# Kernel optimization log

Hardware: AMD Instinct MI355X
Metric: run time of the kernel (lower is better)

## Reference

```python
import jax, jax.numpy as jnp
import numpy as np
import math

N = 200000      # active voxels
M = 100000      # matched in/out pairs per kernel offset
K = 27          # kernel volume (3x3x3)
CIN = 32
COUT = 64


def setup_inputs() -> dict:
    key = jax.random.key(0)
    k1, k2, k3, k4, k5 = jax.random.split(key, 5)
    input_feat = jax.random.normal(k1, (N, CIN), dtype=jnp.float32)
    input_coord = jax.random.randint(k2, (N, 4), 0, 1024, dtype=jnp.int32)
    input_cmap = jax.random.randint(k3, (N,), 0, N, dtype=jnp.int32)
    input_kmap = jax.random.randint(k4, (K, M, 2), 0, N, dtype=jnp.int32)
    std = 1.0 / math.sqrt(CIN * K)  # reset_parameters: uniform(-std, std)
    kw, kb = jax.random.split(k5)
    kernel = jax.random.uniform(kw, (K, CIN, COUT), dtype=jnp.float32,
                                minval=-std, maxval=std)
    bias = jax.random.uniform(kb, (COUT,), dtype=jnp.float32,
                              minval=-std, maxval=std)
    return {"input_feat": input_feat, "input_coord": input_coord,
            "input_cmap": input_cmap, "input_kmap": input_kmap,
            "kernel": kernel, "bias": bias}


def reference(input_feat, input_coord, input_cmap, input_kmap, kernel, bias):
    # Sparse 3D conv, stride=1: output coords == input coords, n_out = N.
    # For each kernel offset k, the kmap gives (in_idx, out_idx) pairs:
    #   out[out_idx] += in[in_idx] @ kernel[k]
    n_out = input_feat.shape[0]
    in_idx = input_kmap[..., 0]           # [K, M]
    out_idx = input_kmap[..., 1]          # [K, M]
    gathered = input_feat[in_idx]         # [K, M, CIN]  (gather)
    contrib = jnp.einsum('kmi,kio->kmo', gathered, kernel)  # per-offset GEMM
    out = jnp.zeros((n_out, kernel.shape[-1]), dtype=input_feat.dtype)
    out = out.at[out_idx.reshape(-1)].add(contrib.reshape(-1, kernel.shape[-1]))
    out = out + bias
    return out
```

## Files before the change

kernel.cpp:

```cpp
#include <hip/hip_runtime.h>

#define KVOL 27
#define CIN  32
#define COUT 64

__global__ __launch_bounds__(256) void init_out_kernel(float* __restrict__ out,
                                                       const float* __restrict__ bias,
                                                       int total4) {
  int i0 = blockIdx.x * 256 + threadIdx.x;
  float4 b = ((const float4*)bias)[i0 & 15];
  for (int i = i0; i < total4; i += gridDim.x * 256) {
    ((float4*)out)[i] = b;
  }
}

__global__ __launch_bounds__(256) void scatter_conv_kernel(
    const float* __restrict__ feat,
    const int2*  __restrict__ kmap,
    const float* __restrict__ kern,
    float*       __restrict__ out,
    int M) {
  const int k    = blockIdx.y;
  const int lane = threadIdx.x & 63;
  const int wave = threadIdx.x >> 6;

  float w[CIN];
  const float* wk = kern + (size_t)k * CIN * COUT + lane;
#pragma unroll
  for (int i = 0; i < CIN; ++i) w[i] = wk[i * COUT];

  const int2* km = kmap + (size_t)k * M;
  const int nwaves = gridDim.x * 4;

  for (int m = blockIdx.x * 4 + wave; m < M; m += nwaves) {
    int2 pr = km[m];
    const float4* frow = (const float4*)(feat + (size_t)pr.x * CIN);
    float acc = 0.f;
#pragma unroll
    for (int j = 0; j < 8; ++j) {
      float4 v = frow[j];
      acc = fmaf(v.x, w[4 * j + 0], acc);
      acc = fmaf(v.y, w[4 * j + 1], acc);
      acc = fmaf(v.z, w[4 * j + 2], acc);
      acc = fmaf(v.w, w[4 * j + 3], acc);
    }
    atomicAdd(out + (size_t)pr.y * COUT + lane, acc);
  }
}

extern "C" void kernel_launch(void* const* d_in, const int* in_sizes, int n_in,
                              void* d_out, int out_size, void* d_ws, size_t ws_size,
                              hipStream_t stream) {
  const float* feat = (const float*)d_in[0];
  const int2*  kmap = (const int2*)d_in[3];
  const float* kern = (const float*)d_in[4];
  const float* bias = (const float*)d_in[5];
  float* out = (float*)d_out;

  const int N = in_sizes[0] / CIN;
  const int M = in_sizes[3] / (2 * KVOL);

  int total4 = N * (COUT / 4);
  int initBlocks = 2048;
  hipLaunchKernelGGL(init_out_kernel, dim3(initBlocks), dim3(256), 0, stream,
                     out, bias, total4);

  dim3 grid(128, KVOL);
  hipLaunchKernelGGL(scatter_conv_kernel, grid, dim3(256), 0, stream,
                     feat, kmap, kern, out, M);
}
```

Baseline: 831.8 us.

## Bin kernel-map pairs by output row and accumulate per tile in LDS

```diff
diff --git a/kernel.cpp b/kernel.cpp
--- a/kernel.cpp
+++ b/kernel.cpp
@@ -1,50 +1,165 @@
 #include <hip/hip_runtime.h>
+#include <stdint.h>
 
 #define KVOL 27
 #define CIN  32
 #define COUT 64
+#define KPG  3
+#define NGRP 9
+#define RB   64
+#define SCAN_CHUNK 4096
 
-__global__ __launch_bounds__(256) void init_out_kernel(float* __restrict__ out,
-                                                       const float* __restrict__ bias,
-                                                       int total4) {
-  int i0 = blockIdx.x * 256 + threadIdx.x;
-  float4 b = ((const float4*)bias)[i0 & 15];
-  for (int i = i0; i < total4; i += gridDim.x * 256) {
-    ((float4*)out)[i] = b;
+__global__ __launch_bounds__(256) void hist_kernel(const int2* __restrict__ kmap,
+                                                   int* __restrict__ count,
+                                                   int M, int N) {
+  int m = blockIdx.x * 256 + threadIdx.x;
+  int k = blockIdx.y;
+  if (m < M) {
+    int out = kmap[(size_t)k * M + m].y;
+    int w = k / KPG;
+    atomicAdd(&count[w * N + out], 1);
   }
 }
 
-__global__ __launch_bounds__(256) void scatter_conv_kernel(
+__global__ __launch_bounds__(256) void scan_reduce(const int* __restrict__ count,
+                                                   int* __restrict__ partial, int nb) {
+  __shared__ int ws[4];
+  int t = threadIdx.x;
+  int base = blockIdx.x * SCAN_CHUNK + t * 16;
+  int s = 0;
+#pragma unroll
+  for (int i = 0; i < 16; ++i) { int idx = base + i; if (idx < nb) s += count[idx]; }
+  for (int d = 32; d; d >>= 1) s += __shfl_down(s, d);
+  if ((t & 63) == 0) ws[t >> 6] = s;
+  __syncthreads();
+  if (t == 0) partial[blockIdx.x] = ws[0] + ws[1] + ws[2] + ws[3];
+}
+
+__global__ __launch_bounds__(64) void scan_partials(int* __restrict__ partial,
+                                                    int nchunks, int* __restrict__ start_nb) {
+  int lane = threadIdx.x;
+  int run = 0;
+  for (int base = 0; base < nchunks; base += 64) {
+    int i = base + lane;
+    int orig = (i < nchunks) ? partial[i] : 0;
+    int v = orig;
+    for (int d = 1; d < 64; d <<= 1) { int u = __shfl_up(v, d); if (lane >= d) v += u; }
+    if (i < nchunks) partial[i] = run + v - orig;
+    run += __shfl(v, 63);
+  }
+  if (lane == 0) *start_nb = run;
+}
+
+__global__ __launch_bounds__(256) void scan_down(const int* __restrict__ count,
+                                                 const int* __restrict__ partial,
+                                                 int* __restrict__ start,
+                                                 int* __restrict__ cursor, int nb) {
+  __shared__ int wsum[4];
+  int t = threadIdx.x, blk = blockIdx.x;
+  int base = blk * SCAN_CHUNK + t * 16;
+  int v[16]; int s = 0;
+#pragma unroll
+  for (int i = 0; i < 16; ++i) { int idx = base + i; v[i] = (idx < nb) ? count[idx] : 0; s += v[i]; }
+  int lane = t & 63, wv = t >> 6;
+  int sv = s;
+  for (int d = 1; d < 64; d <<= 1) { int u = __shfl_up(sv, d); if (lane >= d) sv += u; }
+  if (lane == 63) wsum[wv] = sv;
+  __syncthreads();
+  int wbase = 0;
+  for (int i = 0; i < wv; ++i) wbase += wsum[i];
+  int prefix = partial[blk] + wbase + (sv - s);
+#pragma unroll
+  for (int i = 0; i < 16; ++i) {
+    int idx = base + i;
+    if (idx < nb) { start[idx] = prefix; cursor[idx] = prefix; }
+    prefix += v[i];
+  }
+}
+
+__global__ __launch_bounds__(256) void scatter_kernel(const int2* __restrict__ kmap,
+                                                      int* __restrict__ cursor,
+                                                      uint32_t* __restrict__ binned,
+                                                      int M, int N) {
+  int m = blockIdx.x * 256 + threadIdx.x;
+  int k = blockIdx.y;
+  if (m < M) {
+    int2 p = kmap[(size_t)k * M + m];
+    int w = k / KPG, kl = k - w * KPG;
+    int pos = atomicAdd(&cursor[w * N + p.y], 1);
+    binned[pos] = (uint32_t)p.x | ((uint32_t)kl << 18) | ((uint32_t)(p.y & (RB - 1)) << 20);
+  }
+}
+
+#define DOT32(F, W, ACC) { _Pragma("unroll") \
+  for (int i_ = 0; i_ < CIN; ++i_) ACC = fmaf((F)[i_], W[i_], ACC); }
+
+#define PROC(E) do { \
+  unsigned in_ = (E) & 0x3FFFFu; \
+  int kl_ = ((E) >> 18) & 3; \
+  int rl_ = (int)((E) >> 20); \
+  const float* f_ = feat + (size_t)in_ * CIN; \
+  float acc_ = 0.f; \
+  if (kl_ == 0)      DOT32(f_, w0, acc_) \
+  else if (kl_ == 1) DOT32(f_, w1, acc_) \
+  else               DOT32(f_, w2, acc_) \
+  atomicAdd(&tile[rl_][c], acc_); \
+} while (0)
+
+__global__ __launch_bounds__(NGRP * 64) void gather_out_kernel(
     const float* __restrict__ feat,
-    const int2*  __restrict__ kmap,
+    const uint32_t* __restrict__ binned,
+    const int* __restrict__ start,
     const float* __restrict__ kern,
-    float*       __restrict__ out,
-    int M) {
-  const int k    = blockIdx.y;
-  const int lane = threadIdx.x & 63;
-  const int wave = threadIdx.x >> 6;
+    const float* __restrict__ bias,
+    float* __restrict__ out,
+    int N) {
+  __shared__ float tile[RB][COUT];
+  const int w  = threadIdx.x >> 6;
+  const int c  = threadIdx.x & 63;
+  const int R0 = blockIdx.x * RB;
 
-  float w[CIN];
-  const float* wk = kern + (size_t)k * CIN * COUT + lane;
+  for (int i = threadIdx.x; i < RB * COUT; i += NGRP * 64) ((float*)tile)[i] = 0.f;
+
+  float w0[CIN], w1[CIN], w2[CIN];
+  {
+    const float* kb = kern + (size_t)(w * KPG) * CIN * COUT + c;
 #pragma unroll
-  for (int i = 0; i < CIN; ++i) w[i] = wk[i * COUT];
+    for (int i = 0; i < CIN; ++i) w0[i] = kb[i * COUT];
+#pragma unroll
+    for (int i = 0; i < CIN; ++i) w1[i] = kb[CIN * COUT + i * COUT];
+#pragma unroll
+    for (int i = 0; i < CIN; ++i) w2[i] = kb[2 * CIN * COUT + i * COUT];
+  }
+  __syncthreads();
 
-  const int2* km = kmap + (size_t)k * M;
-  const int nwaves = gridDim.x * 4;
+  const int b0 = w * N + R0;
+  const int s0 = start[b0];
+  const int cnt = start[b0 + RB] - s0;
 
-  for (int m = blockIdx.x * 4 + wave; m < M; m += nwaves) {
-    int2 pr = km[m];
-    const float4* frow = (const float4*)(feat + (size_t)pr.x * CIN);
-    float acc = 0.f;
-#pragma unroll
-    for (int j = 0; j < 8; ++j) {
-      float4 v = frow[j];
-      acc = fmaf(v.x, w[4 * j + 0], acc);
-      acc = fmaf(v.y, w[4 * j + 1], acc);
-      acc = fmaf(v.z, w[4 * j + 2], acc);
-      acc = fmaf(v.w, w[4 * j + 3], acc);
+  for (int base = 0; base < cnt; base += 64) {
+    int idx = base + c;
+    unsigned ent = (idx < cnt) ? binned[s0 + idx] : 0u;
+    int jn = cnt - base; if (jn > 64) jn = 64;
+    int j = 0;
+    for (; j + 2 <= jn; j += 2) {
+      unsigned ea = (unsigned)__builtin_amdgcn_readlane((int)ent, j);
+      unsigned eb = (unsigned)__builtin_amdgcn_readlane((int)ent, j + 1);
+      PROC(ea);
+      PROC(eb);
     }
-    atomicAdd(out + (size_t)pr.y * COUT + lane, acc);
+    if (j < jn) {
+      unsigned ea = (unsigned)__builtin_amdgcn_readlane((int)ent, j);
+      PROC(ea);
+    }
+  }
+  __syncthreads();
+
+  for (int i = threadIdx.x; i < RB * COUT / 4; i += NGRP * 64) {
+    int r = i >> 4, q = i & 15;
+    float4 v = ((float4*)tile[r])[q];
+    float4 b = ((const float4*)bias)[q];
+    v.x += b.x; v.y += b.y; v.z += b.z; v.w += b.w;
+    ((float4*)(out + (size_t)(R0 + r) * COUT))[q] = v;
   }
 }
 
@@ -59,13 +174,26 @@
 
   const int N = in_sizes[0] / CIN;
   const int M = in_sizes[3] / (2 * KVOL);
+  const int E = KVOL * M;
+  const int NB = NGRP * N;
 
-  int total4 = N * (COUT / 4);
-  int initBlocks = 2048;
-  hipLaunchKernelGGL(init_out_kernel, dim3(initBlocks), dim3(256), 0, stream,
-                     out, bias, total4);
+  int* count   = (int*)d_ws;
+  int* start   = count + NB;
+  int* cursor  = start + NB + 1;
+  int* partial = cursor + NB;
+  uint32_t* binned = (uint32_t*)(partial + 4096);
 
-  dim3 grid(128, KVOL);
-  hipLaunchKernelGGL(scatter_conv_kernel, grid, dim3(256), 0, stream,
-                     feat, kmap, kern, out, M);
+  const int nchunks = (NB + SCAN_CHUNK - 1) / SCAN_CHUNK;
+
+  hipMemsetAsync(count, 0, (size_t)NB * sizeof(int), stream);
+
+  dim3 pgrid((M + 255) / 256, KVOL);
+  hipLaunchKernelGGL(hist_kernel, pgrid, dim3(256), 0, stream, kmap, count, M, N);
+  hipLaunchKernelGGL(scan_reduce, dim3(nchunks), dim3(256), 0, stream, count, partial, NB);
+  hipLaunchKernelGGL(scan_partials, dim3(1), dim3(64), 0, stream, partial, nchunks, start + NB);
+  hipLaunchKernelGGL(scan_down, dim3(nchunks), dim3(256), 0, stream,
+                     count, partial, start, cursor, NB);
+  hipLaunchKernelGGL(scatter_kernel, pgrid, dim3(256), 0, stream, kmap, cursor, binned, M, N);
+  hipLaunchKernelGGL(gather_out_kernel, dim3(N / RB), dim3(NGRP * 64), 0, stream,
+                     feat, binned, start, kern, bias, out, N);
 }
```

Result: slower. 1.355 ms (+62.9%).

## Bin kernel-map pairs by output block and accumulate in shared memory

Applied to the files above, without the earlier changes.

```diff
diff --git a/kernel.cpp b/kernel.cpp
--- a/kernel.cpp
+++ b/kernel.cpp
@@ -1,71 +1,129 @@
 #include <hip/hip_runtime.h>
+#include <stdint.h>
 
 #define KVOL 27
 #define CIN  32
 #define COUT 64
+#define RB   32
+#define NWV  4
+#define CAP  48
 
-__global__ __launch_bounds__(256) void init_out_kernel(float* __restrict__ out,
-                                                       const float* __restrict__ bias,
-                                                       int total4) {
-  int i0 = blockIdx.x * 256 + threadIdx.x;
-  float4 b = ((const float4*)bias)[i0 & 15];
-  for (int i = i0; i < total4; i += gridDim.x * 256) {
-    ((float4*)out)[i] = b;
+__global__ __launch_bounds__(256) void binapp_kernel(const int4* __restrict__ kmap2,
+                                                     int* __restrict__ count,
+                                                     uint32_t* __restrict__ binned,
+                                                     int M2) {
+  int t = blockIdx.x * 256 + threadIdx.x;
+  int k = blockIdx.y;
+  if (t < M2) {
+    int4 v = kmap2[(size_t)k * M2 + t];
+    int b1 = (v.y >> 5) * KVOL + k;
+    int p1 = atomicAdd(&count[b1], 1);
+    if (p1 < CAP) binned[(size_t)b1 * CAP + p1] = (uint32_t)v.x | ((uint32_t)(v.y & 31) << 18);
+    int b2 = (v.w >> 5) * KVOL + k;
+    int p2 = atomicAdd(&count[b2], 1);
+    if (p2 < CAP) binned[(size_t)b2 * CAP + p2] = (uint32_t)v.z | ((uint32_t)(v.w & 31) << 18);
   }
 }
 
-__global__ __launch_bounds__(256) void scatter_conv_kernel(
+__global__ __launch_bounds__(256) void conv_dot2(
     const float* __restrict__ feat,
-    const int2*  __restrict__ kmap,
+    const uint32_t* __restrict__ binned,
+    const int* __restrict__ count,
     const float* __restrict__ kern,
-    float*       __restrict__ out,
-    int M) {
-  const int k    = blockIdx.y;
-  const int lane = threadIdx.x & 63;
-  const int wave = threadIdx.x >> 6;
+    const float* __restrict__ bias,
+    float* __restrict__ out) {
+  __shared__ float tile[RB][COUT + 1];
+  const int wv = threadIdx.x >> 6;
+  const int l  = threadIdx.x & 63;
+  const int blk = blockIdx.x;
 
-  float w[CIN];
-  const float* wk = kern + (size_t)k * CIN * COUT + lane;
+  for (int i = threadIdx.x; i < RB * (COUT + 1); i += 256)
+    ((float*)tile)[i] = 0.f;
+  __syncthreads();
+
+  for (int kk = wv; kk < KVOL; kk += NWV) {
+    const int bin = blk * KVOL + kk;
+    int cnt = count[bin]; if (cnt > CAP) cnt = CAP;
+    if (cnt <= 0) continue;
+    const uint32_t* bp = binned + (size_t)bin * CAP;
+
+    float w[CIN];
+    const float* wk = kern + (size_t)kk * CIN * COUT + l;
 #pragma unroll
-  for (int i = 0; i < CIN; ++i) w[i] = wk[i * COUT];
+    for (int i = 0; i < CIN; ++i) w[i] = wk[i * COUT];
 
-  const int2* km = kmap + (size_t)k * M;
-  const int nwaves = gridDim.x * 4;
+    int m = 0;
+    for (; m + 2 <= cnt; m += 2) {
+      uint2 e = *(const uint2*)(bp + m);
+      const float4* f0 = (const float4*)(feat + (size_t)(e.x & 0x3FFFFu) * CIN);
+      const float4* f1 = (const float4*)(feat + (size_t)(e.y & 0x3FFFFu) * CIN);
+      float a0[4] = {0.f, 0.f, 0.f, 0.f};
+      float a1[4] = {0.f, 0.f, 0.f, 0.f};
+#pragma unroll
+      for (int j = 0; j < 8; ++j) {
+        float4 v0 = f0[j];
+        float4 v1 = f1[j];
+        a0[j & 3] = fmaf(v0.x, w[4 * j + 0], a0[j & 3]);
+        a0[j & 3] = fmaf(v0.y, w[4 * j + 1], a0[j & 3]);
+        a0[j & 3] = fmaf(v0.z, w[4 * j + 2], a0[j & 3]);
+        a0[j & 3] = fmaf(v0.w, w[4 * j + 3], a0[j & 3]);
+        a1[j & 3] = fmaf(v1.x, w[4 * j + 0], a1[j & 3]);
+        a1[j & 3] = fmaf(v1.y, w[4 * j + 1], a1[j & 3]);
+        a1[j & 3] = fmaf(v1.z, w[4 * j + 2], a1[j & 3]);
+        a1[j & 3] = fmaf(v1.w, w[4 * j + 3], a1[j & 3]);
+      }
+      float s0 = (a0[0] + a0[1]) + (a0[2] + a0[3]);
+      float s1 = (a1[0] + a1[1]) + (a1[2] + a1[3]);
+      atomicAdd(&tile[(e.x >> 18) & 31][l], s0);
+      atomicAdd(&tile[(e.y >> 18) & 31][l], s1);
+    }
+    if (m < cnt) {
+      uint32_t e0 = bp[m];
+      const float4* f0 = (const float4*)(feat + (size_t)(e0 & 0x3FFFFu) * CIN);
+      float a0[4] = {0.f, 0.f, 0.f, 0.f};
+#pragma unroll
+      for (int j = 0; j < 8; ++j) {
+        float4 v0 = f0[j];
+        a0[j & 3] = fmaf(v0.x, w[4 * j + 0], a0[j & 3]);
+        a0[j & 3] = fmaf(v0.y, w[4 * j + 1], a0[j & 3]);
+        a0[j & 3] = fmaf(v0.z, w[4 * j + 2], a0[j & 3]);
+        a0[j & 3] = fmaf(v0.w, w[4 * j + 3], a0[j & 3]);
+      }
+      atomicAdd(&tile[(e0 >> 18) & 31][l], (a0[0] + a0[1]) + (a0[2] + a0[3]));
+    }
+  }
 
-  for (int m = blockIdx.x * 4 + wave; m < M; m += nwaves) {
-    int2 pr = km[m];
-    const float4* frow = (const float4*)(feat + (size_t)pr.x * CIN);
-    float acc = 0.f;
-#pragma unroll
-    for (int j = 0; j < 8; ++j) {
-      float4 v = frow[j];
-      acc = fmaf(v.x, w[4 * j + 0], acc);
-      acc = fmaf(v.y, w[4 * j + 1], acc);
-      acc = fmaf(v.z, w[4 * j + 2], acc);
-      acc = fmaf(v.w, w[4 * j + 3], acc);
-    }
-    atomicAdd(out + (size_t)pr.y * COUT + lane, acc);
-  }
+  __syncthreads();
+
+  const float bv = bias[l];
+  const int R0 = blk * RB;
+  for (int r = wv; r < RB; r += NWV)
+    out[(size_t)(R0 + r) * COUT + l] = tile[r][l] + bv;
 }
 
 extern "C" void kernel_launch(void* const* d_in, const int* in_sizes, int n_in,
                               void* d_out, int out_size, void* d_ws, size_t ws_size,
                               hipStream_t stream) {
-  const float* feat = (const float*)d_in[0];
-  const int2*  kmap = (const int2*)d_in[3];
-  const float* kern = (const float*)d_in[4];
-  const float* bias = (const float*)d_in[5];
+  const float* feat  = (const float*)d_in[0];
+  const int4*  kmap2 = (const int4*)d_in[3];
+  const float* kern  = (const float*)d_in[4];
+  const float* bias  = (const float*)d_in[5];
   float* out = (float*)d_out;
 
   const int N = in_sizes[0] / CIN;
   const int M = in_sizes[3] / (2 * KVOL);
+  const int M2 = M / 2;
+  const int NB = N / RB;
+  const int NBIN = NB * KVOL;
 
-  int total4 = N * (COUT / 4);
-  int initBlocks = 2048;
-  hipLaunchKernelGGL(init_out_kernel, dim3(initBlocks), dim3(256), 0, stream,
-                     out, bias, total4);
+  int* count = (int*)d_ws;
+  uint32_t* binned = (uint32_t*)(count + NBIN);
 
-  dim3 grid(128, KVOL);
-  hipLaunchKernelGGL(scatter_conv_kernel, grid, dim3(256), 0, stream,
-                     feat, kmap, kern, out, M);
+  hipMemsetAsync(count, 0, (size_t)NBIN * sizeof(int), stream);
+
+  dim3 pgrid((M2 + 255) / 256, KVOL);
+  hipLaunchKernelGGL(binapp_kernel, pgrid, dim3(256), 0, stream, kmap2, count, binned, M2);
+
+  hipLaunchKernelGGL(conv_dot2, dim3(NB), dim3(256), 0, stream,
+                     feat, binned, count, kern, bias, out);
 }
```

Result: slower. 1.118 ms (+34.4%).
